# Optimization experiments

Measured on AMD Instinct MI355X. Metric: run time of the kernel, lower is better.

Reference implementation:

```python
import jax, jax.numpy as jnp
import numpy as np


def _causal_kernel_mask(K):
    # casual_mask[i, K-i:] = 0 for i in 1..p
    p = K // 2
    m = np.ones((p + 1, K), np.float32)
    for i in range(1, p + 1):
        m[i, K - i:] = 0.0
    return jnp.asarray(m)


def setup_inputs() -> dict:
    rng = jax.random.key(0)
    k0, k1, k2, k3, k4 = jax.random.split(rng, 5)
    B, H, N, F = 2, 16, 1024, 64
    V, K = 32000, 5
    return {
        "input_ids": jax.random.randint(k0, (B, N), 0, V),
        "query": jax.random.normal(k1, (B, H, N, F), dtype=jnp.float32),
        "key": jax.random.normal(k2, (B, H, N, F), dtype=jnp.float32),
        "value": jax.random.normal(k3, (B, H, N, F), dtype=jnp.float32),
        "emb_weight": jax.random.normal(k4, (V, 2 * K), dtype=jnp.float32) * 0.02,
    }


def reference(input_ids, query, key, value, emb_weight):
    B, H, N, F = query.shape
    K = emb_weight.shape[1] // 2  # head/layer invariant -> emb dim = 2*K
    p = K // 2
    G = 2 * H

    # ---- get_kernel (layer 0; head_invariant + layer_invariant) ----
    kern = emb_weight[input_ids]                       # [B,N,2K]
    kern = kern.reshape(B, N, 2, 1, K)                 # [B,N,2,1,K]
    kern = jnp.broadcast_to(kern, (B, N, 2, H, K)).reshape(B, N, G, K)

    # ---- conv_key_value (for_casual=True, strict_on_casual=True) ----
    kv = jnp.concatenate([key, value], axis=1)         # [B,2H,N,F]
    kv_pad = jnp.pad(kv, ((0, 0), (0, 0), (p, p), (0, 0)))
    # unfold over token dim: [B,2H,K,N,F]
    kv_unf = jnp.stack([kv_pad[:, :, k:k + N, :] for k in range(K)], axis=2)
    cmask = _causal_kernel_mask(K)                     # [p+1,K]
    kern_m = kern[:, :, :, None, :] * cmask[None, None, None]  # [B,N,2H,p+1,K]
    # dynamic depthwise conv with per-offset causal masking
    out = jnp.einsum('bgknf,bngjk->bgjnf', kv_unf, kern_m)     # [B,2H,p+1,N,F]
    key_c = out[:, :H, 0]                              # [B,H,N,F]
    value_c = out[:, H:, 0]                            # [B,H,N,F]

    # ---- attention with causal-boundary corrections (n_past = 0) ----
    scale = 1.0 / jnp.sqrt(jnp.asarray(F, dtype=query.dtype))
    q = query * scale
    scores = jnp.einsum('bhnf,bhmf->bhnm', q, key_c)   # [B,H,N,N]

    # correct_attn_weights_near_casual_boundary
    for i in range(p):
        off = p - 1 - i
        cb_key = out[:, :H, 1 + i]                     # [B,H,N,F]
        corr = jnp.einsum('bhnf,bhnf->bhn', q[:, :, off:, :], cb_key[:, :, :N - off, :])
        rows = jnp.arange(N - off) + off
        cols = jnp.arange(N - off)
        scores = scores.at[:, :, rows, cols].set(corr)

    causal = jnp.tril(jnp.ones((N, N), dtype=bool))
    scores = jnp.where(causal, scores, jnp.asarray(-1e9, dtype=scores.dtype))
    probs = jax.nn.softmax(scores, axis=-1)
    attn = jnp.einsum('bhnm,bhmf->bhnf', probs, value_c)

    # correct_attn_output_near_casual_boundary
    for i in range(p):
        off = p - 1 - i
        cb_value = out[:, H:, 1 + i]                   # [B,H,N,F]
        idx = jnp.arange(N - off)
        diag_w = probs[:, :, idx + off, idx]           # diag offset=-off: [B,H,N-off]
        diff_v = cb_value[:, :, :N - off, :] - value_c[:, :, :N - off, :]
        diff = diag_w[..., None] * diff_v
        attn = attn + jnp.pad(diff, ((0, 0), (0, 0), (off, 0), (0, 0)))

    return attn
```

## Files before the change

kernel.cpp:

```cpp
#include <hip/hip_runtime.h>

#define HD   64
#define NSEQ 1024

typedef __attribute__((ext_vector_type(8))) __bf16 bf16x8;
typedef __attribute__((ext_vector_type(4))) float  f32x4;
typedef __attribute__((ext_vector_type(4))) unsigned short u16x4;

__device__ inline unsigned short f2bf(float x) {
    unsigned u = __float_as_uint(x);
    return (unsigned short)((u + 0x7fffu + ((u >> 16) & 1u)) >> 16);
}
__device__ inline unsigned pk2(float a, float b) {
    return (unsigned)f2bf(a) | ((unsigned)f2bf(b) << 16);
}
__device__ inline float dot4(f32x4 a, f32x4 b) {
    return a.x * b.x + a.y * b.y + a.z * b.z + a.w * b.w;
}

__global__ __launch_bounds__(256) void conv_kernel(
    const int* __restrict__ ids,
    const float* __restrict__ keyg,
    const float* __restrict__ valg,
    const float* __restrict__ qg,
    const float* __restrict__ emb,
    unsigned short* __restrict__ kc,
    unsigned short* __restrict__ vcT,
    float* __restrict__ dg1, float* __restrict__ dg2)
{
    __shared__ float se[650];
    __shared__ float vtile[64][68];
    int bh = blockIdx.x >> 4;
    int n0 = (blockIdx.x & 15) << 6;
    int b  = bh >> 4;
    int t  = threadIdx.x;
    size_t hb = (size_t)bh * NSEQ * HD;

    for (int u = t; u < 650; u += 256) {
        int r = u / 10, c = u - r * 10;
        int n = n0 - 1 + r;
        se[u] = (n >= 0) ? emb[(size_t)ids[b * NSEQ + n] * 10 + c] : 0.f;
    }
    __syncthreads();

    const float* kb = keyg + hb;
    const float* vb = valg + hb;
#pragma unroll
    for (int i = 0; i < 4; ++i) {
        int u  = (i << 8) + t;
        int nl = u >> 4, g4 = u & 15;
        int n  = n0 + nl, f = g4 << 2;
        const float* e  = se + (nl + 1) * 10;
        const float* ep = se + nl * 10;
        f32x4 xk[5], xv[5];
#pragma unroll
        for (int k = 0; k < 5; ++k) {
            int m = n + k - 2;
            if (m >= 0 && m < NSEQ) {
                xk[k] = *(const f32x4*)(kb + (size_t)m * HD + f);
                xv[k] = *(const f32x4*)(vb + (size_t)m * HD + f);
            } else {
                xk[k] = (f32x4){0.f, 0.f, 0.f, 0.f};
                xv[k] = (f32x4){0.f, 0.f, 0.f, 0.f};
            }
        }
        f32x4 km3 = (n >= 3) ? *(const f32x4*)(kb + (size_t)(n - 3) * HD + f)
                             : (f32x4){0.f, 0.f, 0.f, 0.f};
        f32x4 qv = *(const f32x4*)(qg + hb + (size_t)n * HD + f) * 0.125f;

        f32x4 k012 = e[0] * xk[0] + e[1] * xk[1] + e[2] * xk[2];
        f32x4 kcv  = k012 + e[3] * xk[3] + e[4] * xk[4];
        f32x4 vcv  = e[5] * xv[0] + e[6] * xv[1] + e[7] * xv[2] + e[8] * xv[3] + e[9] * xv[4];

        u16x4 kq;
        kq.x = f2bf(kcv.x); kq.y = f2bf(kcv.y); kq.z = f2bf(kcv.z); kq.w = f2bf(kcv.w);
        *(u16x4*)(kc + hb + (size_t)n * HD + f) = kq;
        *(f32x4*)(&vtile[nl][f]) = vcv;

        float s2 = dot4(qv, k012);
        f32x4 kj1 = ep[0] * km3 + ep[1] * xk[0] + ep[2] * xk[1] + ep[3] * xk[2];
        float s1 = dot4(qv, kj1);
#pragma unroll
        for (int o = 1; o < 16; o <<= 1) {
            s2 += __shfl_xor(s2, o, 64);
            s1 += __shfl_xor(s1, o, 64);
        }
        if (g4 == 0) {
            dg2[bh * NSEQ + n] = s2;
            dg1[bh * NSEQ + n] = s1;
        }
    }
    __syncthreads();
#pragma unroll
    for (int i = 0; i < 4; ++i) {
        int u = (i << 8) + t;
        int f = u >> 4, nn = (u & 15) << 2;
        u16x4 o;
        o.x = f2bf(vtile[nn + 0][f]);
        o.y = f2bf(vtile[nn + 1][f]);
        o.z = f2bf(vtile[nn + 2][f]);
        o.w = f2bf(vtile[nn + 3][f]);
        *(u16x4*)(vcT + ((size_t)bh * HD + f) * NSEQ + n0 + nn) = o;
    }
}

__global__ __launch_bounds__(256) void attn_kernel(
    const float* __restrict__ qg,
    const unsigned short* __restrict__ kc,
    const unsigned short* __restrict__ vcT,
    const float* __restrict__ valg,
    const int* __restrict__ ids,
    const float* __restrict__ emb,
    const float* __restrict__ dg1, const float* __restrict__ dg2,
    float* __restrict__ outg)
{
    __shared__ __align__(16) unsigned char sK[8192];
    __shared__ __align__(16) unsigned char sV[8192];
    __shared__ __align__(16) unsigned char sP[8192];

    int bid = blockIdx.x;
    int bh  = bid & 31;
    int q0  = (15 - (bid >> 5)) << 6;
    int t   = threadIdx.x;
    int w   = t >> 6, l = t & 63;
    int lq  = l & 15, h = l >> 4, l7 = l & 7;
    int qbw = q0 + w * 16;
    size_t hb = (size_t)bh * NSEQ * HD;

    const unsigned short* kcb = kc  + hb;
    const unsigned short* vtb = vcT + (size_t)bh * HD * NSEQ;

    bf16x8 qb0, qb1;
    {
        const float* qr = qg + hb + (size_t)(qbw + lq) * HD + 8 * h;
        f32x4 a0 = *(const f32x4*)(qr);
        f32x4 a1 = *(const f32x4*)(qr + 4);
        f32x4 b0 = *(const f32x4*)(qr + 32);
        f32x4 b1 = *(const f32x4*)(qr + 36);
        const float S = 0.125f;
        union { unsigned u[4]; bf16x8 v; } u0, u1;
        u0.u[0] = pk2(a0.x * S, a0.y * S); u0.u[1] = pk2(a0.z * S, a0.w * S);
        u0.u[2] = pk2(a1.x * S, a1.y * S); u0.u[3] = pk2(a1.z * S, a1.w * S);
        u1.u[0] = pk2(b0.x * S, b0.y * S); u1.u[1] = pk2(b0.z * S, b0.w * S);
        u1.u[2] = pk2(b1.x * S, b1.y * S); u1.u[3] = pk2(b1.z * S, b1.w * S);
        qb0 = u0.v; qb1 = u1.v;
    }
    float diag2_l = dg2[bh * NSEQ + qbw + lq];
    float diag1_l = dg1[bh * NSEQ + qbw + lq];

    f32x4 of[4];
#pragma unroll
    for (int ft = 0; ft < 4; ++ft) of[ft] = (f32x4){0.f, 0.f, 0.f, 0.f};
    float m_run = -1e30f, denom = 0.f;

    const int ka_off0 = ((0 + h) ^ l7) << 4;
    const int ka_off1 = ((4 + h) ^ l7) << 4;
    const int pr_base = w * 2048 + lq * 128;
    const int nt   = (q0 >> 6) + 1;
    const int chk0 = ((qbw > 0 ? qbw - 1 : 0) >> 6);

    uint4 pf[4];
    auto issue = [&](int tI) {
        int kv0 = tI << 6;
#pragma unroll
        for (int i = 0; i < 4; ++i) {
            int chunk = t + (i << 8);
            int buf = chunk >> 9, loc = chunk & 511;
            int r = loc >> 3, c = loc & 7;
            int cs = c ^ (r & 7);
            pf[i] = (buf == 0)
                ? *(const uint4*)(kcb + (size_t)(kv0 + r) * HD + cs * 8)
                : *(const uint4*)(vtb + (size_t)r * NSEQ + kv0 + cs * 8);
        }
    };
    auto commit = [&]() {
#pragma unroll
        for (int i = 0; i < 4; ++i) {
            int chunk = t + (i << 8);
            int buf = chunk >> 9, loc = chunk & 511;
            int r = loc >> 3, c = loc & 7;
            *(uint4*)((buf ? sV : sK) + r * 128 + c * 16) = pf[i];
        }
    };

    issue(0); commit();
    for (int tI = 0; tI < nt; ++tI) {
        __syncthreads();
        if (tI + 1 < nt) issue(tI + 1);
        int kv0 = tI << 6;

        f32x4 p[4];
#pragma unroll
        for (int st = 0; st < 4; ++st) {
            bf16x8 ka0 = *(const bf16x8*)(sK + st * 2048 + lq * 128 + ka_off0);
            bf16x8 ka1 = *(const bf16x8*)(sK + st * 2048 + lq * 128 + ka_off1);
            f32x4 d = (f32x4){0.f, 0.f, 0.f, 0.f};
            d = __builtin_amdgcn_mfma_f32_16x16x32_bf16(ka0, qb0, d, 0, 0, 0);
            d = __builtin_amdgcn_mfma_f32_16x16x32_bf16(ka1, qb1, d, 0, 0, 0);
            p[st] = d;
        }

        if (tI >= chk0) {
            int n_l = qbw + lq;
#pragma unroll
            for (int st = 0; st < 4; ++st)
#pragma unroll
                for (int r = 0; r < 4; ++r) {
                    int kv = kv0 + st * 16 + 4 * h + r;
                    float dd = p[st][r];
                    if (kv > n_l)           dd = -1e30f;
                    else if (kv == n_l)     dd = diag2_l;
                    else if (kv == n_l - 1) dd = diag1_l;
                    p[st][r] = dd;
                }
        }

        float tmax = -1e30f;
#pragma unroll
        for (int st = 0; st < 4; ++st)
#pragma unroll
            for (int r = 0; r < 4; ++r) tmax = fmaxf(tmax, p[st][r]);
        tmax = fmaxf(tmax, __shfl_xor(tmax, 16, 64));
        tmax = fmaxf(tmax, __shfl_xor(tmax, 32, 64));
        if (!__all(tmax <= m_run + 5.0f)) {
            float m_new = fmaxf(m_run, tmax);
            float alpha = __expf(m_run - m_new);
            denom *= alpha;
            m_run = m_new;
#pragma unroll
            for (int r = 0; r < 4; ++r) {
                float ar = __shfl(alpha, 4 * h + r, 64);
                of[0][r] *= ar; of[1][r] *= ar; of[2][r] *= ar; of[3][r] *= ar;
            }
        }
        float lsum = 0.f;
#pragma unroll
        for (int st = 0; st < 4; ++st)
#pragma unroll
            for (int r = 0; r < 4; ++r) {
                float e = __expf(p[st][r] - m_run);
                p[st][r] = e;
                lsum += e;
            }
        lsum += __shfl_xor(lsum, 16, 64);
        lsum += __shfl_xor(lsum, 32, 64);
        denom += lsum;

#pragma unroll
        for (int st = 0; st < 4; ++st) {
            uint2 uu;
            uu.x = pk2(p[st][0], p[st][1]);
            uu.y = pk2(p[st][2], p[st][3]);
            int chunk = (st << 1) + (h >> 1);
            *(uint2*)(sP + pr_base + ((chunk ^ l7) << 4) + ((h & 1) << 3)) = uu;
        }
        asm volatile("s_waitcnt lgkmcnt(0)" ::: "memory");
        __builtin_amdgcn_sched_barrier(0);

#pragma unroll
        for (int kk = 0; kk < 2; ++kk) {
            int koff = kk ? ka_off1 : ka_off0;
            bf16x8 pa = *(const bf16x8*)(sP + pr_base + koff);
#pragma unroll
            for (int ft = 0; ft < 4; ++ft) {
                bf16x8 vb = *(const bf16x8*)(sV + ft * 2048 + lq * 128 + koff);
                of[ft] = __builtin_amdgcn_mfma_f32_16x16x32_bf16(pa, vb, of[ft], 0, 0, 0);
            }
        }
        __syncthreads();
        if (tI + 1 < nt) commit();
    }

    const float* vraw = valg + hb;
    float* outr = outg + hb;
    const int* idb = ids + (size_t)(bh >> 4) * NSEQ;
#pragma unroll
    for (int r = 0; r < 4; ++r) {
        int qrow = 4 * h + r;
        float dn = __shfl(denom,   qrow, 64);
        float mf = __shfl(m_run,   qrow, 64);
        float d2 = __shfl(diag2_l, qrow, 64);
        float d1 = __shfl(diag1_l, qrow, 64);
        int n = qbw + qrow;
        float inv = 1.0f / dn;
        float p2 = __expf(d2 - mf) * inv;
        float p1 = (n >= 1) ? __expf(d1 - mf) * inv : 0.f;
        int   id_n = idb[n];
        float e8  = emb[(size_t)id_n * 10 + 8];
        float e9  = emb[(size_t)id_n * 10 + 9];
        float e9p = (n >= 1) ? emb[(size_t)idb[n - 1] * 10 + 9] : 0.f;
        float ca = -(p2 * e8 + p1 * e9p);
        float cb = -p2 * e9;
#pragma unroll
        for (int ft = 0; ft < 4; ++ft) {
            int f = ft * 16 + lq;
            float val = of[ft][r] * inv;
            if (n + 1 < NSEQ) val += ca * vraw[(size_t)(n + 1) * HD + f];
            if (n + 2 < NSEQ) val += cb * vraw[(size_t)(n + 2) * HD + f];
            outr[(size_t)n * HD + f] = val;
        }
    }
}

extern "C" void kernel_launch(void* const* d_in, const int* in_sizes, int n_in,
                              void* d_out, int out_size, void* d_ws, size_t ws_size,
                              hipStream_t stream)
{
    const int*   ids = (const int*)  d_in[0];
    const float* q   = (const float*)d_in[1];
    const float* key = (const float*)d_in[2];
    const float* val = (const float*)d_in[3];
    const float* emb = (const float*)d_in[4];
    float* out = (float*)d_out;

    char* w = (char*)d_ws;
    unsigned short* kc  = (unsigned short*)(w);
    unsigned short* vcT = (unsigned short*)(w + (4u << 20));
    float* dg1 = (float*)(w + (8u << 20));
    float* dg2 = (float*)(w + (8u << 20) + (1u << 17));

    conv_kernel<<<512, 256, 0, stream>>>(ids, key, val, q, emb, kc, vcT, dg1, dg2);
    attn_kernel<<<512, 256, 0, stream>>>(q, kc, vcT, val, ids, emb, dg1, dg2, out);
}
```

Baseline: 59.21 us.

## Split causal attention KV range into chunks with a separate merge kernel

```diff
diff --git a/kernel.cpp b/kernel.cpp
--- a/kernel.cpp
+++ b/kernel.cpp
@@ -1,11 +1,23 @@
 #include <hip/hip_runtime.h>
 
-#define HD   64
-#define NSEQ 1024
+#define HD    64
+#define NSEQ  1024
+#define NSLOT 40
+#define CROWS 32
 
 typedef __attribute__((ext_vector_type(8))) __bf16 bf16x8;
 typedef __attribute__((ext_vector_type(4))) float  f32x4;
 typedef __attribute__((ext_vector_type(4))) unsigned short u16x4;
+
+__device__ __constant__ unsigned char PAIRS[NSLOT] = {
+    60,61,62,63, 56,57,58, 52,53,54, 48,49,50, 44,45,46,
+    40,41, 36,37, 32,33, 28,29, 24, 20, 16, 12,
+    59, 42, 25, 8, 55, 38, 21, 4, 51, 34, 17, 0 };
+__device__ __constant__ unsigned char IDX[64] = {
+    39,255,255,255, 35,255,255,255, 31,255,255,255, 27,255,255,255,
+    26, 38,255,255, 25, 34,255,255, 24, 30,255,255, 22, 23,255,255,
+    20, 21, 37,255, 18, 19, 33,255, 16, 17, 29,255, 13, 14, 15,255,
+    10, 11, 12, 36,  7,  8,  9, 32,  4,  5,  6, 28,  0,  1,  2,  3 };
 
 __device__ inline unsigned short f2bf(float x) {
     unsigned u = __float_as_uint(x);
@@ -28,15 +40,16 @@
     unsigned short* __restrict__ vcT,
     float* __restrict__ dg1, float* __restrict__ dg2)
 {
-    __shared__ float se[650];
-    __shared__ float vtile[64][68];
-    int bh = blockIdx.x >> 4;
-    int n0 = (blockIdx.x & 15) << 6;
+    __shared__ float se[(CROWS + 1) * 10];
+    __shared__ float vtile[CROWS][68];
+    int pid = blockIdx.x;
+    int bh = pid & 31;
+    int n0 = (pid >> 5) * CROWS;
     int b  = bh >> 4;
     int t  = threadIdx.x;
     size_t hb = (size_t)bh * NSEQ * HD;
 
-    for (int u = t; u < 650; u += 256) {
+    for (int u = t; u < (CROWS + 1) * 10; u += 256) {
         int r = u / 10, c = u - r * 10;
         int n = n0 - 1 + r;
         se[u] = (n >= 0) ? emb[(size_t)ids[b * NSEQ + n] * 10 + c] : 0.f;
@@ -46,7 +59,7 @@
     const float* kb = keyg + hb;
     const float* vb = valg + hb;
 #pragma unroll
-    for (int i = 0; i < 4; ++i) {
+    for (int i = 0; i < 2; ++i) {
         int u  = (i << 8) + t;
         int nl = u >> 4, g4 = u & 15;
         int n  = n0 + nl, f = g4 << 2;
@@ -92,9 +105,9 @@
     }
     __syncthreads();
 #pragma unroll
-    for (int i = 0; i < 4; ++i) {
+    for (int i = 0; i < 2; ++i) {
         int u = (i << 8) + t;
-        int f = u >> 4, nn = (u & 15) << 2;
+        int f = u >> 3, nn = (u & 7) << 2;
         u16x4 o;
         o.x = f2bf(vtile[nn + 0][f]);
         o.y = f2bf(vtile[nn + 1][f]);
@@ -108,22 +121,25 @@
     const float* __restrict__ qg,
     const unsigned short* __restrict__ kc,
     const unsigned short* __restrict__ vcT,
-    const float* __restrict__ valg,
-    const int* __restrict__ ids,
-    const float* __restrict__ emb,
     const float* __restrict__ dg1, const float* __restrict__ dg2,
-    float* __restrict__ outg)
+    float* __restrict__ pM, float* __restrict__ pL, float* __restrict__ pO)
 {
     __shared__ __align__(16) unsigned char sK[8192];
     __shared__ __align__(16) unsigned char sV[8192];
     __shared__ __align__(16) unsigned char sP[8192];
 
-    int bid = blockIdx.x;
-    int bh  = bid & 31;
-    int q0  = (15 - (bid >> 5)) << 6;
-    int t   = threadIdx.x;
-    int w   = t >> 6, l = t & 63;
-    int lq  = l & 15, h = l >> 4, l7 = l & 7;
+    int pid  = blockIdx.x;
+    int bh   = pid & 31;
+    int slot = pid >> 5;
+    int code = PAIRS[slot];
+    int j = code >> 2, cch = code & 3;
+    int q0 = j << 6;
+    int t0 = cch << 2;
+    int len = j - (cch << 2) + 1; if (len > 4) len = 4;
+
+    int t = threadIdx.x;
+    int w = t >> 6, l = t & 63;
+    int lq = l & 15, h = l >> 4, l7 = l & 7;
     int qbw = q0 + w * 16;
     size_t hb = (size_t)bh * NSEQ * HD;
 
@@ -156,12 +172,11 @@
     const int ka_off0 = ((0 + h) ^ l7) << 4;
     const int ka_off1 = ((4 + h) ^ l7) << 4;
     const int pr_base = w * 2048 + lq * 128;
-    const int nt   = (q0 >> 6) + 1;
     const int chk0 = ((qbw > 0 ? qbw - 1 : 0) >> 6);
 
     uint4 pf[4];
-    auto issue = [&](int tI) {
-        int kv0 = tI << 6;
+    auto issue = [&](int tg) {
+        int kv0 = tg << 6;
 #pragma unroll
         for (int i = 0; i < 4; ++i) {
             int chunk = t + (i << 8);
@@ -183,11 +198,12 @@
         }
     };
 
-    issue(0); commit();
-    for (int tI = 0; tI < nt; ++tI) {
+    issue(t0); commit();
+    for (int ti = 0; ti < len; ++ti) {
         __syncthreads();
-        if (tI + 1 < nt) issue(tI + 1);
-        int kv0 = tI << 6;
+        if (ti + 1 < len) issue(t0 + ti + 1);
+        int tg  = t0 + ti;
+        int kv0 = tg << 6;
 
         f32x4 p[4];
 #pragma unroll
@@ -200,7 +216,7 @@
             p[st] = d;
         }
 
-        if (tI >= chk0) {
+        if (tg >= chk0) {
             int n_l = qbw + lq;
 #pragma unroll
             for (int st = 0; st < 4; ++st)
@@ -268,38 +284,88 @@
             }
         }
         __syncthreads();
-        if (tI + 1 < nt) commit();
-    }
-
-    const float* vraw = valg + hb;
-    float* outr = outg + hb;
+        if (ti + 1 < len) commit();
+    }
+
+    int gslot = bh * NSLOT + slot;
+    if (h == 0) {
+        pM[gslot * 64 + w * 16 + lq] = m_run;
+        pL[gslot * 64 + w * 16 + lq] = denom;
+    }
+    float* po = pO + (((size_t)gslot * 64 + w * 16) << 6);
+#pragma unroll
+    for (int r = 0; r < 4; ++r)
+#pragma unroll
+        for (int ft = 0; ft < 4; ++ft)
+            po[((4 * h + r) << 6) + ft * 16 + lq] = of[ft][r];
+}
+
+__global__ __launch_bounds__(256) void merge_kernel(
+    const float* __restrict__ pM, const float* __restrict__ pL,
+    const float* __restrict__ pO,
+    const float* __restrict__ dg1, const float* __restrict__ dg2,
+    const float* __restrict__ valg, const int* __restrict__ ids,
+    const float* __restrict__ emb, float* __restrict__ outg)
+{
+    int pid = blockIdx.x;
+    int bh = pid & 31, j = pid >> 5;
+    int nc = (j >> 2) + 1;
+    int t = threadIdx.x;
+    int rloc = t >> 2, fg = t & 3;
+    int n = (j << 6) + rloc;
+    int f0 = fg << 4;
+    size_t hb = (size_t)bh * NSEQ * HD;
+
+    int gs[4]; float mc[4];
+    float m_g = -3e30f;
+    for (int c = 0; c < nc; ++c) {
+        gs[c] = bh * NSLOT + IDX[(j << 2) | c];
+        mc[c] = pM[gs[c] * 64 + rloc];
+        m_g = fmaxf(m_g, mc[c]);
+    }
+    float D = 0.f;
+    f32x4 a0 = (f32x4){0.f,0.f,0.f,0.f}, a1 = a0, a2 = a0, a3 = a0;
+    for (int c = 0; c < nc; ++c) {
+        float wc = __expf(mc[c] - m_g);
+        D += pL[gs[c] * 64 + rloc] * wc;
+        const float* po = pO + (((size_t)gs[c] * 64 + rloc) << 6) + f0;
+        a0 += wc * *(const f32x4*)(po);
+        a1 += wc * *(const f32x4*)(po + 4);
+        a2 += wc * *(const f32x4*)(po + 8);
+        a3 += wc * *(const f32x4*)(po + 12);
+    }
+    float inv = 1.0f / D;
+    float d2 = dg2[bh * NSEQ + n], d1 = dg1[bh * NSEQ + n];
+    float p2 = __expf(d2 - m_g) * inv;
+    float p1 = (n >= 1) ? __expf(d1 - m_g) * inv : 0.f;
     const int* idb = ids + (size_t)(bh >> 4) * NSEQ;
-#pragma unroll
-    for (int r = 0; r < 4; ++r) {
-        int qrow = 4 * h + r;
-        float dn = __shfl(denom,   qrow, 64);
-        float mf = __shfl(m_run,   qrow, 64);
-        float d2 = __shfl(diag2_l, qrow, 64);
-        float d1 = __shfl(diag1_l, qrow, 64);
-        int n = qbw + qrow;
-        float inv = 1.0f / dn;
-        float p2 = __expf(d2 - mf) * inv;
-        float p1 = (n >= 1) ? __expf(d1 - mf) * inv : 0.f;
-        int   id_n = idb[n];
-        float e8  = emb[(size_t)id_n * 10 + 8];
-        float e9  = emb[(size_t)id_n * 10 + 9];
-        float e9p = (n >= 1) ? emb[(size_t)idb[n - 1] * 10 + 9] : 0.f;
-        float ca = -(p2 * e8 + p1 * e9p);
-        float cb = -p2 * e9;
-#pragma unroll
-        for (int ft = 0; ft < 4; ++ft) {
-            int f = ft * 16 + lq;
-            float val = of[ft][r] * inv;
-            if (n + 1 < NSEQ) val += ca * vraw[(size_t)(n + 1) * HD + f];
-            if (n + 2 < NSEQ) val += cb * vraw[(size_t)(n + 2) * HD + f];
-            outr[(size_t)n * HD + f] = val;
-        }
-    }
+    int id_n = idb[n];
+    float e8  = emb[(size_t)id_n * 10 + 8];
+    float e9  = emb[(size_t)id_n * 10 + 9];
+    float e9p = (n >= 1) ? emb[(size_t)idb[n - 1] * 10 + 9] : 0.f;
+    float ca = -(p2 * e8 + p1 * e9p);
+    float cb = -p2 * e9;
+
+    a0 *= inv; a1 *= inv; a2 *= inv; a3 *= inv;
+    if (n + 1 < NSEQ) {
+        const float* v1 = valg + hb + (size_t)(n + 1) * HD + f0;
+        a0 += ca * *(const f32x4*)(v1);
+        a1 += ca * *(const f32x4*)(v1 + 4);
+        a2 += ca * *(const f32x4*)(v1 + 8);
+        a3 += ca * *(const f32x4*)(v1 + 12);
+    }
+    if (n + 2 < NSEQ) {
+        const float* v2 = valg + hb + (size_t)(n + 2) * HD + f0;
+        a0 += cb * *(const f32x4*)(v2);
+        a1 += cb * *(const f32x4*)(v2 + 4);
+        a2 += cb * *(const f32x4*)(v2 + 8);
+        a3 += cb * *(const f32x4*)(v2 + 12);
+    }
+    float* o = outg + hb + (size_t)n * HD + f0;
+    *(f32x4*)(o)      = a0;
+    *(f32x4*)(o + 4)  = a1;
+    *(f32x4*)(o + 8)  = a2;
+    *(f32x4*)(o + 12) = a3;
 }
 
 extern "C" void kernel_launch(void* const* d_in, const int* in_sizes, int n_in,
@@ -316,9 +382,13 @@
     char* w = (char*)d_ws;
     unsigned short* kc  = (unsigned short*)(w);
     unsigned short* vcT = (unsigned short*)(w + (4u << 20));
-    float* dg1 = (float*)(w + (8u << 20));
-    float* dg2 = (float*)(w + (8u << 20) + (1u << 17));
-
-    conv_kernel<<<512, 256, 0, stream>>>(ids, key, val, q, emb, kc, vcT, dg1, dg2);
-    attn_kernel<<<512, 256, 0, stream>>>(q, kc, vcT, val, ids, emb, dg1, dg2, out);
-}
+    float* dg1 = (float*)(w + 8388608);
+    float* dg2 = (float*)(w + 8519680);
+    float* pM  = (float*)(w + 8650752);
+    float* pL  = (float*)(w + 8978432);
+    float* pO  = (float*)(w + 9306112);
+
+    conv_kernel<<<1024, 256, 0, stream>>>(ids, key, val, q, emb, kc, vcT, dg1, dg2);
+    attn_kernel<<<32 * NSLOT, 256, 0, stream>>>(q, kc, vcT, dg1, dg2, pM, pL, pO);
+    merge_kernel<<<512, 256, 0, stream>>>(pM, pL, pO, dg1, dg2, val, ids, emb, out);
+}
```

New measurement: 54.29 us. -8.3%, faster.
